# Optimization experiments

Measured on AMD Instinct MI355X. Metric: run time of the kernel, lower is better.

Reference implementation:

```python
import jax, jax.numpy as jnp
import numpy as np

B, C, D, E = 2048, 64, 1024, 128
P_INT = 0.0  # p_int=0 -> intervention mask is all zeros (deterministic)


def setup_inputs() -> dict:
    key = jax.random.key(0)
    ks = jax.random.split(key, 16)
    s = lambda k, shape, fan: jax.random.normal(k, shape, jnp.float32) * (1.0 / np.sqrt(fan))
    return {
        "x": jax.random.normal(ks[0], (B, D), jnp.float32),
        "c_int": jax.random.uniform(ks[1], (B, C), jnp.float32),
        # stacked per-concept scorer MLP: Linear(D,D) -> ReLU -> Linear(D,1) -> Sigmoid
        "W1": s(ks[2], (C, D, D), D), "b1": jnp.zeros((C, D), jnp.float32),
        "w2": s(ks[3], (C, D), D), "b2": jnp.zeros((C,), jnp.float32),
        # stacked per-concept embed layer: Linear(D+1, D+1) -> ReLU
        "Wl": s(ks[4], (C, D + 1, D + 1), D + 1), "bl": jnp.zeros((C, D + 1), jnp.float32),
        # shared heads
        "Wmu": s(ks[5], (D + 1, E), D + 1), "bmu": jnp.zeros((E,), jnp.float32),
        "Wlv": s(ks[6], (D + 1, E), D + 1), "blv": jnp.zeros((E,), jnp.float32),
        "proto_pos": jax.random.normal(ks[7], (C, E), jnp.float32),
        "proto_neg": jax.random.normal(ks[8], (C, E), jnp.float32),
    }


def reference(x, c_int, W1, b1, w2, b2, Wl, bl, Wmu, bmu, Wlv, blv, proto_pos, proto_neg):
    # Concept scorers (all concepts batched as one grouped GEMM).
    h = jax.nn.relu(jnp.einsum("bd,cdk->bck", x, W1) + b1)          # [B,C,D]
    c_pred = jax.nn.sigmoid(jnp.einsum("bck,ck->bc", h, w2) + b2)    # [B,C]
    # Per-concept embedding layer on [x ; c_pred].
    xc = jnp.concatenate(
        [jnp.broadcast_to(x[:, None, :], (x.shape[0], C, D)), c_pred[..., None]], axis=-1
    )                                                                # [B,C,D+1]
    emb = jax.nn.relu(jnp.einsum("bck,ckj->bcj", xc, Wl) + bl)       # [B,C,D+1]
    mu = jnp.einsum("bcj,je->bce", emb, Wmu) + bmu                   # [B,C,E]
    logvar = jnp.einsum("bcj,je->bce", emb, Wlv) + blv               # [B,C,E]
    c_emb = mu  # eval mode: no reparameterization noise
    # Intervention blend (mask ~ Bernoulli(p_int); p_int=0 -> zeros, deterministic)
    mask = jnp.zeros_like(c_pred)                                    # [B,C]
    cp = mask * c_int + (1.0 - mask) * c_pred                        # [B,C]
    proto = cp[..., None] * proto_pos + (1.0 - cp[..., None]) * proto_neg  # [B,C,E]
    c_emb = mask[..., None] * proto + (1.0 - mask[..., None]) * c_emb
    return (c_pred, c_emb, mu, logvar)
```

## Files before the change

kernel.cpp:

```cpp
#include <hip/hip_runtime.h>
#include <hip/hip_bf16.h>
#include <cstdint>
#include <cstddef>

#define OFF_CE 131072ull
#define OFF_MU (131072ull + 16777216ull)
#define OFF_LV (131072ull + 33554432ull)

using bf16x8 = __attribute__((ext_vector_type(8))) __bf16;
using s16x8  = __attribute__((ext_vector_type(8))) short;
using f32x4  = __attribute__((ext_vector_type(4))) float;

__device__ __forceinline__ unsigned short f2bf(float x) {
  unsigned u = __builtin_bit_cast(unsigned, x);
  return (unsigned short)((u + 0x7FFFu + ((u >> 16) & 1u)) >> 16);
}
__device__ __forceinline__ float bf2f(unsigned short h) {
  unsigned u = ((unsigned)h) << 16;
  return __builtin_bit_cast(float, u);
}
__device__ __forceinline__ void async16(const void* g, void* l) {
  __builtin_amdgcn_global_load_lds(
      (const __attribute__((address_space(1))) void*)g,
      (__attribute__((address_space(3))) void*)l, 16, 0, 0);
}

struct P2 {
  const float *b2, *presum, *w2l, *bl1024;
  float *e1024, *pred;
};

template <int ALIGNED>
__device__ __forceinline__ void tile_tr64(const float* __restrict__ src, int stride,
                                          unsigned short* __restrict__ dst, int tid,
                                          float (*t)[68]) {
#pragma unroll
  for (int i = 0; i < 4; ++i) {
    const int row = (tid >> 4) + (i << 4);
    const int col4 = (tid & 15) << 2;
    const float* sp = src + (size_t)row * stride + col4;
    float4 v;
    if constexpr (ALIGNED) {
      v = *(const float4*)sp;
    } else {
      v.x = sp[0]; v.y = sp[1]; v.z = sp[2]; v.w = sp[3];
    }
    *(float4*)&t[row][col4] = v;
  }
  __syncthreads();
  const int n = tid & 63;
#pragma unroll
  for (int p = 0; p < 2; ++p) {
    const int k8 = ((tid >> 6) << 3) + (p << 5);
    unsigned short tmp[8];
#pragma unroll
    for (int j = 0; j < 8; ++j) tmp[j] = f2bf(t[k8 + j][n]);
    *(uint4*)(dst + (size_t)n * 1024 + k8) = *(uint4*)tmp;
  }
}

__global__ __launch_bounds__(256) void prep1_k(const float* __restrict__ W1,
                                               const float* __restrict__ x,
                                               const float* __restrict__ Wl,
                                               const float* __restrict__ bl,
                                               unsigned short* __restrict__ xb,
                                               unsigned short* __restrict__ W1T,
                                               float* __restrict__ wlastf,
                                               float* __restrict__ blpf,
                                               float* __restrict__ Wlcolf,
                                               float* __restrict__ w2l,
                                               float* __restrict__ bl1024) {
  __shared__ float t[64][68];
  const int bid = blockIdx.x;
  const int tid = threadIdx.x;
  if (bid < 16384) {
    const int c = bid >> 8, kt = (bid >> 4) & 15, nt = bid & 15;
    tile_tr64<1>(W1 + ((size_t)c << 20) + ((size_t)(kt << 6) << 10) + (nt << 6), 1024,
                 W1T + ((size_t)c << 20) + ((size_t)(nt << 6) << 10) + (kt << 6), tid, t);
  } else if (bid < 17408) {
    const int idx = (bid - 16384) * 256 + tid;
    const float4* xv = (const float4*)x;
    float4 a = xv[idx * 2], b = xv[idx * 2 + 1];
    unsigned w0 = f2bf(a.x) | ((unsigned)f2bf(a.y) << 16);
    unsigned w1 = f2bf(a.z) | ((unsigned)f2bf(a.w) << 16);
    unsigned w2 = f2bf(b.x) | ((unsigned)f2bf(b.y) << 16);
    unsigned w3 = f2bf(b.z) | ((unsigned)f2bf(b.w) << 16);
    ((uint4*)xb)[idx] = make_uint4(w0, w1, w2, w3);
  } else {
    const int idx = (bid - 17408) * 256 + tid;
    const int c = idx >> 10, j = idx & 1023;
    const float* src = Wl + (size_t)c * 1050625;
    wlastf[idx] = src[(size_t)1024 * 1025 + j];
    blpf[idx]   = bl[(size_t)c * 1025 + j];
    Wlcolf[idx] = src[(size_t)j * 1025 + 1024];
    if (j == 0) {
      w2l[c]    = src[(size_t)1024 * 1025 + 1024];
      bl1024[c] = bl[(size_t)c * 1025 + 1024];
    }
  }
}

__global__ __launch_bounds__(256) void wl2_k(const float* __restrict__ Wl,
                                             const float* __restrict__ Wmu,
                                             const float* __restrict__ Wlv,
                                             const unsigned short* __restrict__ xb,
                                             const float* __restrict__ Wlcolf,
                                             unsigned short* __restrict__ WlT,
                                             unsigned short* __restrict__ WheadT,
                                             float* __restrict__ whead1024f,
                                             float* __restrict__ presum) {
  __shared__ float t[64][68];
  const int bid = blockIdx.x;
  const int tid = threadIdx.x;
  if (bid < 16384) {
    const int c = bid >> 8, kt = (bid >> 4) & 15, nt = bid & 15;
    tile_tr64<0>(Wl + (size_t)c * 1050625 + (size_t)(kt << 6) * 1025 + (nt << 6), 1025,
                 WlT + ((size_t)c << 20) + ((size_t)(nt << 6) << 10) + (kt << 6), tid, t);
  } else if (bid < 17408) {
    const int e = bid - 16384;
    const int idx = e * 256 + tid;
    const int rr = idx >> 10, k = idx & 1023;
    float v = (rr < 128) ? Wmu[(size_t)k * 128 + rr] : Wlv[(size_t)k * 128 + (rr - 128)];
    WheadT[idx] = f2bf(v);
    if (e == 0)
      whead1024f[tid] = (tid < 128) ? Wmu[131072 + tid] : Wlv[131072 + (tid - 128)];
  } else {
    const int b = bid - 17408;
    const int w = tid >> 6, lane = tid & 63;
    const unsigned short* xr = xb + ((size_t)b << 10) + lane * 16;
    s16x8 xv0 = *(const s16x8*)xr;
    s16x8 xv1 = *(const s16x8*)(xr + 8);
    float xf[16];
#pragma unroll
    for (int i = 0; i < 8; ++i) {
      xf[i] = bf2f((unsigned short)xv0[i]);
      xf[8 + i] = bf2f((unsigned short)xv1[i]);
    }
#pragma unroll
    for (int t16 = 0; t16 < 16; ++t16) {
      const int c = (t16 << 2) + w;
      const float* wr = Wlcolf + (c << 10) + lane * 16;
      float s = 0.f;
#pragma unroll
      for (int q = 0; q < 4; ++q) {
        float4 wv = *(const float4*)(wr + q * 4);
        s += xf[q * 4 + 0] * wv.x + xf[q * 4 + 1] * wv.y +
             xf[q * 4 + 2] * wv.z + xf[q * 4 + 3] * wv.w;
      }
#pragma unroll
      for (int off = 32; off; off >>= 1) s += __shfl_xor(s, off);
      if (lane == 0) presum[(c << 11) + b] = s;
    }
  }
}


#define BAR() __builtin_amdgcn_s_barrier()
#define LGKM0() do { asm volatile("s_waitcnt lgkmcnt(0)" ::: "memory"); \
                     __builtin_amdgcn_sched_barrier(0); } while (0)
#define VM4() asm volatile("s_waitcnt vmcnt(4)" ::: "memory")
#define VM0() asm volatile("s_waitcnt vmcnt(0)" ::: "memory")

#define STAGEA(h, tt, bidx) do { _Pragma("unroll") for (int q_ = 0; q_ < 2; ++q_) \
  async16(Asrc[q_] + ((size_t)(h) * 128) * K + (size_t)(tt) * 64, \
          &sA[bidx][(h) * 8192 + chnk[q_]]); } while (0)
#define STAGEB(h, tt, bidx) do { _Pragma("unroll") for (int q_ = 0; q_ < 2; ++q_) \
  async16(Bsrc[q_] + ((size_t)(h) * 128) * K + (size_t)(tt) * 64, \
          &sB[bidx][(h) * 8192 + chnk[q_]]); } while (0)

#define LOADA(mh, bidx) do { _Pragma("unroll") for (int i_ = 0; i_ < 4; ++i_) { \
  const int ro_ = ((mh) * 128 + wm64 + i_ * 16 + l15) << 6; \
  a[i_][0] = *(const bf16x8*)&sA[bidx][ro_ + ccx0]; \
  a[i_][1] = *(const bf16x8*)&sA[bidx][ro_ + ccx1]; } } while (0)

#define LOADB(nh, bb, bidx) do { _Pragma("unroll") for (int j_ = 0; j_ < 2; ++j_) { \
  const int ro_ = ((nh) * 128 + wn32 + j_ * 16 + l15) << 6; \
  bb[j_][0] = *(const bf16x8*)&sB[bidx][ro_ + ccx0]; \
  bb[j_][1] = *(const bf16x8*)&sB[bidx][ro_ + ccx1]; } } while (0)

#define MMAQ(mh, nh, bb) do { _Pragma("unroll") for (int i_ = 0; i_ < 4; ++i_) \
  _Pragma("unroll") for (int j_ = 0; j_ < 2; ++j_) { \
    acc[(mh)*4+i_][(nh)*2+j_] = __builtin_amdgcn_mfma_f32_16x16x32_bf16( \
        a[i_][0], bb[j_][0], acc[(mh)*4+i_][(nh)*2+j_], 0, 0, 0); \
    acc[(mh)*4+i_][(nh)*2+j_] = __builtin_amdgcn_mfma_f32_16x16x32_bf16( \
        a[i_][1], bb[j_][1], acc[(mh)*4+i_][(nh)*2+j_], 0, 0, 0); \
  } } while (0)

template <int MODE>
__global__ __launch_bounds__(512, 2) void gemm8p_k(
    const unsigned short* __restrict__ A, const unsigned short* __restrict__ BT, const int K,
    const float* __restrict__ e0, const float* __restrict__ e1,
    const float* __restrict__ e2, const float* __restrict__ e3,
    unsigned short* __restrict__ obf, float* __restrict__ ofl, P2 p) {
  __shared__ unsigned short sA[2][16384];
  __shared__ unsigned short sB[2][16384];

  constexpr int GX = (MODE == 2) ? 1 : 4;
  constexpr int GY = (MODE == 2) ? 512 : 8;
  constexpr int NWG = GX * GY * ((MODE == 2) ? 1 : 64);

  const int tid = threadIdx.x;
  const int lane = tid & 63;
  const int wid = tid >> 6;
  const int wm = wid >> 2, wn = wid & 3;
  const int l15 = lane & 15, l4 = lane >> 4;
  const int wm64 = wm << 6, wn32 = wn << 5;

  const int rbid = blockIdx.x + GX * (blockIdx.y + GY * blockIdx.z);
  const int bid = (rbid & 7) * (NWG >> 3) + (rbid >> 3);
  const int bx = bid % GX;
  const int by = (bid / GX) % GY;
  const int c = bid / (GX * GY);

  const int n0 = bx << 8;
  const int m0 = by << 8;

  const unsigned short* Ab = A;
  const unsigned short* Bb;
  if constexpr (MODE == 2) Bb = BT;
  else                     Bb = BT + ((size_t)c << 20);

  int rloc[2], csrc[2], chnk[2];
  const unsigned short* Asrc[2];
  const unsigned short* Bsrc[2];
#pragma unroll
  for (int q = 0; q < 2; ++q) {
    const int s = ((wid << 1) + q) * 64 + lane;
    rloc[q] = s >> 3;
    csrc[q] = ((s & 7) ^ ((s >> 3) & 7)) << 3;
    chnk[q] = ((wid << 1) + q) << 9;
    Asrc[q] = Ab + (size_t)(m0 + rloc[q]) * K + csrc[q];
    Bsrc[q] = Bb + (size_t)(n0 + rloc[q]) * K + csrc[q];
  }

  const int xorv = l15 & 7;
  const int ccx0 = (l4 ^ xorv) << 3;
  const int ccx1 = ((4 + l4) ^ xorv) << 3;

  f32x4 acc[8][4];
#pragma unroll
  for (int i = 0; i < 8; ++i)
#pragma unroll
    for (int j = 0; j < 4; ++j) acc[i][j] = (f32x4)(0.f);

  bf16x8 a[4][2], b0[2][2], b1[2][2];

  const int nt = K >> 6;

  STAGEA(0, 0, 0); STAGEB(0, 0, 0); STAGEB(1, 0, 0); STAGEA(1, 0, 0);
  VM0();
  BAR();

  for (int t = 0; t < nt - 1; ++t) {
    const int cb = t & 1, nb = cb ^ 1;
    LOADA(0, cb);
    LOADB(0, b0, cb);
    STAGEA(0, t + 1, nb);
    BAR();
    LGKM0();
    __builtin_amdgcn_s_setprio(1);
    MMAQ(0, 0, b0);
    __builtin_amdgcn_s_setprio(0);
    VM4();
    BAR();
    LOADB(1, b1, cb);
    STAGEB(0, t + 1, nb);
    BAR();
    LGKM0();
    __builtin_amdgcn_s_setprio(1);
    MMAQ(0, 1, b1);
    __builtin_amdgcn_s_setprio(0);
    VM4();
    BAR();
    LOADA(1, cb);
    STAGEB(1, t + 1, nb);
    BAR();
    LGKM0();
    __builtin_amdgcn_s_setprio(1);
    MMAQ(1, 1, b1);
    __builtin_amdgcn_s_setprio(0);
    BAR();
    STAGEA(1, t + 1, nb);
    BAR();
    __builtin_amdgcn_s_setprio(1);
    MMAQ(1, 0, b0);
    __builtin_amdgcn_s_setprio(0);
    VM4();
    BAR();
  }

  {
    const int cb = (nt - 1) & 1;
    VM0();
    BAR();
    LOADA(0, cb);
    LOADB(0, b0, cb);
    LGKM0();
    __builtin_amdgcn_s_setprio(1);
    MMAQ(0, 0, b0);
    __builtin_amdgcn_s_setprio(0);
    LOADB(1, b1, cb);
    LGKM0();
    __builtin_amdgcn_s_setprio(1);
    MMAQ(0, 1, b1);
    __builtin_amdgcn_s_setprio(0);
    LOADA(1, cb);
    LGKM0();
    __builtin_amdgcn_s_setprio(1);
    MMAQ(1, 1, b1);
    MMAQ(1, 0, b0);
    __builtin_amdgcn_s_setprio(0);
  }

  int coln[2][2];
#pragma unroll
  for (int nh = 0; nh < 2; ++nh)
#pragma unroll
    for (int j = 0; j < 2; ++j) coln[nh][j] = n0 + nh * 128 + wn32 + j * 16 + l15;

  if constexpr (MODE == 0) {
    float bias[2][2], w2v[2][2];
#pragma unroll
    for (int nh = 0; nh < 2; ++nh)
#pragma unroll
      for (int j = 0; j < 2; ++j) {
        bias[nh][j] = e0[(c << 10) + coln[nh][j]];
        w2v[nh][j]  = e1[(c << 10) + coln[nh][j]];
      }
    float* partL = (float*)&sA[0][0];
#pragma unroll
    for (int mh = 0; mh < 2; ++mh)
#pragma unroll
      for (int i = 0; i < 4; ++i)
#pragma unroll
        for (int rr = 0; rr < 4; ++rr) {
          float s = 0.f;
#pragma unroll
          for (int nh = 0; nh < 2; ++nh)
#pragma unroll
            for (int j = 0; j < 2; ++j) {
              float v = fmaxf(acc[mh * 4 + i][nh * 2 + j][rr] + bias[nh][j], 0.f);
              s += v * w2v[nh][j];
            }
          s += __shfl_xor(s, 1); s += __shfl_xor(s, 2);
          s += __shfl_xor(s, 4); s += __shfl_xor(s, 8);
          if (l15 == 0) partL[wid * 128 + mh * 64 + i * 16 + (l4 << 2) + rr] = s;
        }
    __syncthreads();
    if (tid < 256) {
      const int r = tid;
      const int mh_ = r >> 7, wmr = (r >> 6) & 1, low = r & 63;
      float s2 = 0.f;
#pragma unroll
      for (int wn2 = 0; wn2 < 4; ++wn2) s2 += partL[(wmr * 4 + wn2) * 128 + mh_ * 64 + low];
      ofl[(((size_t)(bx << 6) + c) << 11) + m0 + r] = s2;
    }
  } else if constexpr (MODE == 1) {
    float* cpL = (float*)&sA[0][0];
    if (tid < 256) {
      const int b = m0 + tid;
      float s = p.b2[c];
#pragma unroll
      for (int q = 0; q < 4; ++q) s += e2[(((size_t)(q << 6) + c) << 11) + b];
      float pv = 1.f / (1.f + expf(-s));
      cpL[tid] = pv;
      if (bx == 0) {
        p.pred[((size_t)b << 6) + c] = pv;
        p.e1024[(c << 11) + b] =
            fmaxf(p.presum[(c << 11) + b] + pv * p.w2l[c] + p.bl1024[c], 0.f);
      }
    }
    __syncthreads();
    float wl4[2][2], bb4[2][2];
#pragma unroll
    for (int nh = 0; nh < 2; ++nh)
#pragma unroll
      for (int j = 0; j < 2; ++j) {
        wl4[nh][j] = e0[(c << 10) + coln[nh][j]];
        bb4[nh][j] = e1[(c << 10) + coln[nh][j]];
      }
#pragma unroll
    for (int mh = 0; mh < 2; ++mh)
#pragma unroll
      for (int i = 0; i < 4; ++i)
#pragma unroll
        for (int rr = 0; rr < 4; ++rr) {
          const int rl = mh * 128 + wm64 + i * 16 + (l4 << 2) + rr;
          const int row = m0 + rl;
          const float cp = cpL[rl];
          unsigned short* orow = obf + (((size_t)(c << 11) + row) << 10);
#pragma unroll
          for (int nh = 0; nh < 2; ++nh)
#pragma unroll
            for (int j = 0; j < 2; ++j) {
              float v = acc[mh * 4 + i][nh * 2 + j][rr] + cp * wl4[nh][j] + bb4[nh][j];
              orow[coln[nh][j]] = f2bf(fmaxf(v, 0.f));
            }
        }
  } else {
    float bias[2][2], wh[2][2];
#pragma unroll
    for (int nh = 0; nh < 2; ++nh)
#pragma unroll
      for (int j = 0; j < 2; ++j) {
        bias[nh][j] = (nh == 0) ? e0[coln[0][j]] : e1[coln[1][j] - 128];
        wh[nh][j]   = e3[coln[nh][j]];
      }
#pragma unroll
    for (int mh = 0; mh < 2; ++mh)
#pragma unroll
      for (int i = 0; i < 4; ++i)
#pragma unroll
        for (int rr = 0; rr < 4; ++rr) {
          const int rid = m0 + mh * 128 + wm64 + i * 16 + (l4 << 2) + rr;
          const int cc = rid >> 11, b = rid & 2047;
          const float ev = e2[rid];
          const size_t ib = (((size_t)b << 6) + cc) << 7;
#pragma unroll
          for (int j = 0; j < 2; ++j) {
            float v = acc[mh * 4 + i][j][rr] + bias[0][j] + ev * wh[0][j];
            ofl[OFF_MU + ib + coln[0][j]] = v;
            ofl[OFF_CE + ib + coln[0][j]] = v;
          }
#pragma unroll
          for (int j = 0; j < 2; ++j) {
            float v = acc[mh * 4 + i][2 + j][rr] + bias[1][j] + ev * wh[1][j];
            ofl[OFF_LV + ib + (coln[1][j] - 128)] = v;
          }
        }
  }
}


extern "C" void kernel_launch(void* const* d_in, const int* in_sizes, int n_in,
                              void* d_out, int out_size, void* d_ws, size_t ws_size,
                              hipStream_t stream) {
  const float* x   = (const float*)d_in[0];
  const float* W1  = (const float*)d_in[2];
  const float* b1  = (const float*)d_in[3];
  const float* w2  = (const float*)d_in[4];
  const float* b2  = (const float*)d_in[5];
  const float* Wl  = (const float*)d_in[6];
  const float* bl  = (const float*)d_in[7];
  const float* Wmu = (const float*)d_in[8];
  const float* bmu = (const float*)d_in[9];
  const float* Wlv = (const float*)d_in[10];
  const float* blv = (const float*)d_in[11];
  float* out = (float*)d_out;

  char* ws = (char*)d_ws;
  size_t off = 0;
  auto take = [&](size_t bytes) { char* r = ws + off; off += bytes; return r; };
  unsigned short* xb     = (unsigned short*)take(4194304);
  unsigned short* WT     = (unsigned short*)take(134217728);
  float* wlastf          = (float*)take(262144);
  float* blpf            = (float*)take(262144);
  float* Wlcolf          = (float*)take(262144);
  float* w2l             = (float*)take(512);
  float* bl1024          = (float*)take(512);
  unsigned short* WheadT = (unsigned short*)take(524288);
  float* whead1024f      = (float*)take(1024);
  float* presum          = (float*)take(524288);
  float* spart           = (float*)take(2097152);
  float* e1024f          = (float*)take(524288);
  unsigned short* emb    = (unsigned short*)take(268435456);

  P2 p;
  p.b2 = b2; p.presum = presum; p.w2l = w2l; p.bl1024 = bl1024;
  p.e1024 = e1024f; p.pred = out;

  prep1_k<<<17664, 256, 0, stream>>>(W1, x, Wl, bl, xb, WT, wlastf, blpf, Wlcolf, w2l, bl1024);
  gemm8p_k<0><<<dim3(4, 8, 64), 512, 0, stream>>>(xb, WT, 1024, b1, w2, nullptr, nullptr,
                                                  nullptr, spart, p);
  wl2_k<<<19456, 256, 0, stream>>>(Wl, Wmu, Wlv, xb, Wlcolf, WT, WheadT, whead1024f, presum);
  gemm8p_k<1><<<dim3(4, 8, 64), 512, 0, stream>>>(xb, WT, 1024, wlastf, blpf, spart, nullptr,
                                                  emb, nullptr, p);
  gemm8p_k<2><<<dim3(1, 512, 1), 512, 0, stream>>>(emb, WheadT, 1024, bmu, blv, e1024f,
                                                   whead1024f, nullptr, out, p);
}
```

Baseline: 992.1 us.

## Fuse Wl transpose and tail prep into first GEMM launch as extra blocks

Removes the separate wl2_k launch and appends its work (head weight transpose, presum dot products, Wl tile transposes) as trailing blocks of the MODE 0 GEMM grid. Those blocks then overlap with the W1 grouped GEMM, and one kernel boundary disappears. To allow this, W1T and WlT now get separate workspace buffers. It also turns K into a compile-time constant with a fully scheduled K loop, and uses nontemporal loads for the Wl transpose. The costs are an extra 128MB of workspace and tail blocks that compete with the GEMM for CUs and bandwidth.

```diff
diff --git a/kernel.cpp b/kernel.cpp
--- a/kernel.cpp
+++ b/kernel.cpp
@@ -25,33 +25,40 @@
       (__attribute__((address_space(3))) void*)l, 16, 0, 0);
 }
 
-struct P2 {
-  const float *b2, *presum, *w2l, *bl1024;
-  float *e1024, *pred;
+struct PX {
+  const float *Wl, *Wmu, *Wlv, *b2, *presum, *w2l, *bl1024, *Wlcolf;
+  const unsigned short *xb;
+  unsigned short *WlT, *WheadT;
+  float *whead1024f, *e1024, *pred;
 };
 
-template <int ALIGNED>
+template <int ALIGNED, int NT>
 __device__ __forceinline__ void tile_tr64(const float* __restrict__ src, int stride,
-                                          unsigned short* __restrict__ dst, int tid,
+                                          unsigned short* __restrict__ dst, int t256,
                                           float (*t)[68]) {
 #pragma unroll
   for (int i = 0; i < 4; ++i) {
-    const int row = (tid >> 4) + (i << 4);
-    const int col4 = (tid & 15) << 2;
+    const int row = (t256 >> 4) + (i << 4);
+    const int col4 = (t256 & 15) << 2;
     const float* sp = src + (size_t)row * stride + col4;
     float4 v;
     if constexpr (ALIGNED) {
       v = *(const float4*)sp;
+    } else if constexpr (NT) {
+      v.x = __builtin_nontemporal_load(sp);
+      v.y = __builtin_nontemporal_load(sp + 1);
+      v.z = __builtin_nontemporal_load(sp + 2);
+      v.w = __builtin_nontemporal_load(sp + 3);
     } else {
       v.x = sp[0]; v.y = sp[1]; v.z = sp[2]; v.w = sp[3];
     }
     *(float4*)&t[row][col4] = v;
   }
   __syncthreads();
-  const int n = tid & 63;
-#pragma unroll
-  for (int p = 0; p < 2; ++p) {
-    const int k8 = ((tid >> 6) << 3) + (p << 5);
+  const int n = t256 & 63;
+#pragma unroll
+  for (int pq = 0; pq < 2; ++pq) {
+    const int k8 = ((t256 >> 6) << 3) + (pq << 5);
     unsigned short tmp[8];
 #pragma unroll
     for (int j = 0; j < 8; ++j) tmp[j] = f2bf(t[k8 + j][n]);
@@ -75,8 +82,8 @@
   const int tid = threadIdx.x;
   if (bid < 16384) {
     const int c = bid >> 8, kt = (bid >> 4) & 15, nt = bid & 15;
-    tile_tr64<1>(W1 + ((size_t)c << 20) + ((size_t)(kt << 6) << 10) + (nt << 6), 1024,
-                 W1T + ((size_t)c << 20) + ((size_t)(nt << 6) << 10) + (kt << 6), tid, t);
+    tile_tr64<1, 0>(W1 + ((size_t)c << 20) + ((size_t)(kt << 6) << 10) + (nt << 6), 1024,
+                    W1T + ((size_t)c << 20) + ((size_t)(nt << 6) << 10) + (kt << 6), tid, t);
   } else if (bid < 17408) {
     const int idx = (bid - 16384) * 256 + tid;
     const float4* xv = (const float4*)x;
@@ -100,34 +107,20 @@
   }
 }
 
-__global__ __launch_bounds__(256) void wl2_k(const float* __restrict__ Wl,
-                                             const float* __restrict__ Wmu,
-                                             const float* __restrict__ Wlv,
-                                             const unsigned short* __restrict__ xb,
-                                             const float* __restrict__ Wlcolf,
-                                             unsigned short* __restrict__ WlT,
-                                             unsigned short* __restrict__ WheadT,
-                                             float* __restrict__ whead1024f,
-                                             float* __restrict__ presum) {
-  __shared__ float t[64][68];
-  const int bid = blockIdx.x;
-  const int tid = threadIdx.x;
-  if (bid < 16384) {
-    const int c = bid >> 8, kt = (bid >> 4) & 15, nt = bid & 15;
-    tile_tr64<0>(Wl + (size_t)c * 1050625 + (size_t)(kt << 6) * 1025 + (nt << 6), 1025,
-                 WlT + ((size_t)c << 20) + ((size_t)(nt << 6) << 10) + (kt << 6), tid, t);
-  } else if (bid < 17408) {
-    const int e = bid - 16384;
-    const int idx = e * 256 + tid;
+__device__ void tail_work(int e, int tid, char* lds, const PX& p) {
+  if (e < 512) {
+    const int idx = e * 512 + tid;
     const int rr = idx >> 10, k = idx & 1023;
-    float v = (rr < 128) ? Wmu[(size_t)k * 128 + rr] : Wlv[(size_t)k * 128 + (rr - 128)];
-    WheadT[idx] = f2bf(v);
-    if (e == 0)
-      whead1024f[tid] = (tid < 128) ? Wmu[131072 + tid] : Wlv[131072 + (tid - 128)];
-  } else {
-    const int b = bid - 17408;
+    float v = (rr < 128) ? p.Wmu[(size_t)k * 128 + rr] : p.Wlv[(size_t)k * 128 + (rr - 128)];
+    p.WheadT[idx] = f2bf(v);
+    if (e == 0 && tid < 256)
+      p.whead1024f[tid] = (tid < 128) ? p.Wmu[131072 + tid] : p.Wlv[131072 + (tid - 128)];
+    return;
+  }
+  if (e < 2560) {
+    const int b = e - 512;
     const int w = tid >> 6, lane = tid & 63;
-    const unsigned short* xr = xb + ((size_t)b << 10) + lane * 16;
+    const unsigned short* xr = p.xb + ((size_t)b << 10) + lane * 16;
     s16x8 xv0 = *(const s16x8*)xr;
     s16x8 xv1 = *(const s16x8*)(xr + 8);
     float xf[16];
@@ -137,21 +130,29 @@
       xf[8 + i] = bf2f((unsigned short)xv1[i]);
     }
 #pragma unroll
-    for (int t16 = 0; t16 < 16; ++t16) {
-      const int c = (t16 << 2) + w;
-      const float* wr = Wlcolf + (c << 10) + lane * 16;
+    for (int q = 0; q < 8; ++q) {
+      const int c = (q << 3) + w;
+      const float* wr = p.Wlcolf + (c << 10) + lane * 16;
       float s = 0.f;
 #pragma unroll
-      for (int q = 0; q < 4; ++q) {
-        float4 wv = *(const float4*)(wr + q * 4);
-        s += xf[q * 4 + 0] * wv.x + xf[q * 4 + 1] * wv.y +
-             xf[q * 4 + 2] * wv.z + xf[q * 4 + 3] * wv.w;
+      for (int q4 = 0; q4 < 4; ++q4) {
+        float4 wv = *(const float4*)(wr + q4 * 4);
+        s += xf[q4 * 4 + 0] * wv.x + xf[q4 * 4 + 1] * wv.y +
+             xf[q4 * 4 + 2] * wv.z + xf[q4 * 4 + 3] * wv.w;
       }
 #pragma unroll
       for (int off = 32; off; off >>= 1) s += __shfl_xor(s, off);
-      if (lane == 0) presum[(c << 11) + b] = s;
-    }
-  }
+      if (lane == 0) ((float*)p.presum)[(c << 11) + b] = s;
+    }
+    return;
+  }
+  const int u = e - 2560;
+  const int half = tid >> 8, t256 = tid & 255;
+  const int tau = (u << 1) + half;
+  const int c = tau >> 8, kt = (tau >> 4) & 15, ntl = tau & 15;
+  float (*t)[68] = (float(*)[68])(lds + half * (64 * 68 * 4));
+  tile_tr64<0, 1>(p.Wl + (size_t)c * 1050625 + (size_t)(kt << 6) * 1025 + (ntl << 6), 1025,
+                  p.WlT + ((size_t)c << 20) + ((size_t)(ntl << 6) << 10) + (kt << 6), t256, t);
 }
 
 
@@ -186,12 +187,31 @@
         a[i_][1], bb[j_][1], acc[(mh)*4+i_][(nh)*2+j_], 0, 0, 0); \
   } } while (0)
 
-template <int MODE>
+#define KSTEP(t_, cb_, nb_) do { \
+    LOADA(0, cb_); LOADB(0, b0, cb_); STAGEA(0, (t_) + 1, nb_); \
+    BAR(); LGKM0(); \
+    __builtin_amdgcn_s_setprio(1); MMAQ(0, 0, b0); __builtin_amdgcn_s_setprio(0); \
+    VM4(); BAR(); \
+    LOADB(1, b1, cb_); STAGEB(0, (t_) + 1, nb_); \
+    BAR(); LGKM0(); \
+    __builtin_amdgcn_s_setprio(1); MMAQ(0, 1, b1); __builtin_amdgcn_s_setprio(0); \
+    VM4(); BAR(); \
+    LOADA(1, cb_); STAGEB(1, (t_) + 1, nb_); \
+    BAR(); LGKM0(); \
+    __builtin_amdgcn_s_setprio(1); MMAQ(1, 1, b1); __builtin_amdgcn_s_setprio(0); \
+    BAR(); \
+    STAGEA(1, (t_) + 1, nb_); \
+    BAR(); \
+    __builtin_amdgcn_s_setprio(1); MMAQ(1, 0, b0); __builtin_amdgcn_s_setprio(0); \
+    VM4(); BAR(); \
+  } while (0)
+
+template <int MODE, int K>
 __global__ __launch_bounds__(512, 2) void gemm8p_k(
-    const unsigned short* __restrict__ A, const unsigned short* __restrict__ BT, const int K,
+    const unsigned short* __restrict__ A, const unsigned short* __restrict__ BT,
     const float* __restrict__ e0, const float* __restrict__ e1,
     const float* __restrict__ e2, const float* __restrict__ e3,
-    unsigned short* __restrict__ obf, float* __restrict__ ofl, P2 p) {
+    unsigned short* __restrict__ obf, float* __restrict__ ofl, PX p) {
   __shared__ unsigned short sA[2][16384];
   __shared__ unsigned short sB[2][16384];
 
@@ -200,13 +220,22 @@
   constexpr int NWG = GX * GY * ((MODE == 2) ? 1 : 64);
 
   const int tid = threadIdx.x;
+
+  int rbid;
+  if constexpr (MODE == 0) {
+    const int bidR = blockIdx.x;
+    if (bidR >= 2048) { tail_work(bidR - 2048, tid, (char*)&sA[0][0], p); return; }
+    rbid = bidR;
+  } else {
+    rbid = blockIdx.x + GX * (blockIdx.y + GY * blockIdx.z);
+  }
+
   const int lane = tid & 63;
   const int wid = tid >> 6;
   const int wm = wid >> 2, wn = wid & 3;
   const int l15 = lane & 15, l4 = lane >> 4;
   const int wm64 = wm << 6, wn32 = wn << 5;
 
-  const int rbid = blockIdx.x + GX * (blockIdx.y + GY * blockIdx.z);
   const int bid = (rbid & 7) * (NWG >> 3) + (rbid >> 3);
   const int bx = bid % GX;
   const int by = (bid / GX) % GY;
@@ -245,66 +274,35 @@
 
   bf16x8 a[4][2], b0[2][2], b1[2][2];
 
-  const int nt = K >> 6;
+  static_assert(K == 1024, "schedule assumes 16 K-tiles");
 
   STAGEA(0, 0, 0); STAGEB(0, 0, 0); STAGEB(1, 0, 0); STAGEA(1, 0, 0);
   VM0();
   BAR();
 
-  for (int t = 0; t < nt - 1; ++t) {
-    const int cb = t & 1, nb = cb ^ 1;
-    LOADA(0, cb);
-    LOADB(0, b0, cb);
-    STAGEA(0, t + 1, nb);
+#pragma unroll 1
+  for (int tt = 0; tt < 7; ++tt) {
+    const int t0 = tt << 1;
+    KSTEP(t0, 0, 1);
+    KSTEP(t0 + 1, 1, 0);
+  }
+  KSTEP(14, 0, 1);
+
+  {
+    VM0();
     BAR();
+    LOADA(0, 1);
+    LOADB(0, b0, 1);
     LGKM0();
     __builtin_amdgcn_s_setprio(1);
     MMAQ(0, 0, b0);
     __builtin_amdgcn_s_setprio(0);
-    VM4();
-    BAR();
-    LOADB(1, b1, cb);
-    STAGEB(0, t + 1, nb);
-    BAR();
+    LOADB(1, b1, 1);
     LGKM0();
     __builtin_amdgcn_s_setprio(1);
     MMAQ(0, 1, b1);
     __builtin_amdgcn_s_setprio(0);
-    VM4();
-    BAR();
-    LOADA(1, cb);
-    STAGEB(1, t + 1, nb);
-    BAR();
-    LGKM0();
-    __builtin_amdgcn_s_setprio(1);
-    MMAQ(1, 1, b1);
-    __builtin_amdgcn_s_setprio(0);
-    BAR();
-    STAGEA(1, t + 1, nb);
-    BAR();
-    __builtin_amdgcn_s_setprio(1);
-    MMAQ(1, 0, b0);
-    __builtin_amdgcn_s_setprio(0);
-    VM4();
-    BAR();
-  }
-
-  {
-    const int cb = (nt - 1) & 1;
-    VM0();
-    BAR();
-    LOADA(0, cb);
-    LOADB(0, b0, cb);
-    LGKM0();
-    __builtin_amdgcn_s_setprio(1);
-    MMAQ(0, 0, b0);
-    __builtin_amdgcn_s_setprio(0);
-    LOADB(1, b1, cb);
-    LGKM0();
-    __builtin_amdgcn_s_setprio(1);
-    MMAQ(0, 1, b1);
-    __builtin_amdgcn_s_setprio(0);
-    LOADA(1, cb);
+    LOADA(1, 1);
     LGKM0();
     __builtin_amdgcn_s_setprio(1);
     MMAQ(1, 1, b1);
@@ -452,7 +450,8 @@
   size_t off = 0;
   auto take = [&](size_t bytes) { char* r = ws + off; off += bytes; return r; };
   unsigned short* xb     = (unsigned short*)take(4194304);
-  unsigned short* WT     = (unsigned short*)take(134217728);
+  unsigned short* W1T    = (unsigned short*)take(134217728);
+  unsigned short* WlT    = (unsigned short*)take(134217728);
   float* wlastf          = (float*)take(262144);
   float* blpf            = (float*)take(262144);
   float* Wlcolf          = (float*)take(262144);
@@ -465,16 +464,17 @@
   float* e1024f          = (float*)take(524288);
   unsigned short* emb    = (unsigned short*)take(268435456);
 
-  P2 p;
-  p.b2 = b2; p.presum = presum; p.w2l = w2l; p.bl1024 = bl1024;
-  p.e1024 = e1024f; p.pred = out;
-
-  prep1_k<<<17664, 256, 0, stream>>>(W1, x, Wl, bl, xb, WT, wlastf, blpf, Wlcolf, w2l, bl1024);
-  gemm8p_k<0><<<dim3(4, 8, 64), 512, 0, stream>>>(xb, WT, 1024, b1, w2, nullptr, nullptr,
-                                                  nullptr, spart, p);
-  wl2_k<<<19456, 256, 0, stream>>>(Wl, Wmu, Wlv, xb, Wlcolf, WT, WheadT, whead1024f, presum);
-  gemm8p_k<1><<<dim3(4, 8, 64), 512, 0, stream>>>(xb, WT, 1024, wlastf, blpf, spart, nullptr,
-                                                  emb, nullptr, p);
-  gemm8p_k<2><<<dim3(1, 512, 1), 512, 0, stream>>>(emb, WheadT, 1024, bmu, blv, e1024f,
-                                                   whead1024f, nullptr, out, p);
-}
+  PX p;
+  p.Wl = Wl; p.Wmu = Wmu; p.Wlv = Wlv; p.b2 = b2;
+  p.presum = presum; p.w2l = w2l; p.bl1024 = bl1024; p.Wlcolf = Wlcolf;
+  p.xb = xb; p.WlT = WlT; p.WheadT = WheadT;
+  p.whead1024f = whead1024f; p.e1024 = e1024f; p.pred = out;
+
+  prep1_k<<<17664, 256, 0, stream>>>(W1, x, Wl, bl, xb, W1T, wlastf, blpf, Wlcolf, w2l, bl1024);
+  gemm8p_k<0, 1024><<<12800, 512, 0, stream>>>(xb, W1T, b1, w2, nullptr, nullptr,
+                                               nullptr, spart, p);
+  gemm8p_k<1, 1024><<<dim3(4, 8, 64), 512, 0, stream>>>(xb, WlT, wlastf, blpf, spart, nullptr,
+                                                        emb, nullptr, p);
+  gemm8p_k<2, 1024><<<dim3(1, 512, 1), 512, 0, stream>>>(emb, WheadT, bmu, blv, e1024f,
+                                                         whead1024f, nullptr, out, p);
+}
```

Result: faster. 952.1 us (-4.0%).
